# Performance work log

Hardware: AMD Instinct MI355X
Metric: run time of the kernel (lower is better)

## Reference

```python
import jax, jax.numpy as jnp
import numpy as np

B, S, D, DFF = 4, 2048, 1024, 4096


def setup_inputs() -> dict:
    key = jax.random.key(0)
    ks = jax.random.split(key, 7)
    scale = 1.0 / np.sqrt(D)
    return {
        "x": jax.random.normal(ks[0], (B, S, D), dtype=jnp.float32),
        "wq": jax.random.normal(ks[1], (D, D), dtype=jnp.float32) * scale,
        "wk": jax.random.normal(ks[2], (D, D), dtype=jnp.float32) * scale,
        "wv": jax.random.normal(ks[3], (D, D), dtype=jnp.float32) * scale,
        "wo": jax.random.normal(ks[4], (D, D), dtype=jnp.float32) * scale,
        "w1": jax.random.normal(ks[5], (D, DFF), dtype=jnp.float32) * scale,
        "w2": jax.random.normal(ks[6], (DFF, D), dtype=jnp.float32) * (1.0 / np.sqrt(DFF)),
    }


def reference(x, wq, wk, wv, wo, w1, w2):
    # Single-head attention, NO 1/sqrt(d) scaling (faithful to source).
    q = x @ wq  # [B,S,D]
    k = x @ wk
    v = x @ wv
    scores = jnp.einsum("bsd,btd->bst", q, k)  # [B,S,S]
    weights = jax.nn.softmax(scores, axis=-1)
    attn = jnp.einsum("bst,btd->bsd", weights, v)
    proj = attn @ wo
    hidden = jax.nn.relu(proj @ w1)  # [B,S,DFF]
    out = hidden @ w2
    return out + x
```

## Files before the change

kernel.cpp:

```cpp
#include <hip/hip_runtime.h>
#include <hip/hip_bf16.h>
#include <hip/hip_fp16.h>


typedef _Float16 f16;
typedef __attribute__((ext_vector_type(8))) _Float16 f16x8;
typedef __attribute__((ext_vector_type(4))) _Float16 f16x4;
typedef __attribute__((ext_vector_type(4))) float f32x4;

#define BM 128
#define BN 128
#define BK 64

__device__ inline void gload16(const void* g, void* l) {
    __builtin_amdgcn_global_load_lds(
        (const __attribute__((address_space(1))) void*)g,
        (__attribute__((address_space(3))) void*)l, 16, 0, 0);
}

template<int EPI>
__global__ __launch_bounds__(256, 2)
void gemm_f16(const f16* __restrict__ A, const f16* __restrict__ Bt,
              const float* __restrict__ Res, void* __restrict__ Cv,
              int K, int lda, int ldb, int ldc,
              long long sA, long long sB, long long sC)
{
    __shared__ char smem[32 * 1024];
    f16* Ash = (f16*)smem;
    f16* Bsh = (f16*)(smem + 16384);
    float* xbuf = (float*)smem;

    const int t = threadIdx.x;
    const int z = blockIdx.z;
    A  += (size_t)z * sA;
    Bt += (size_t)z * sB;

    const int bm0 = blockIdx.x * BM;
    const int bn0 = blockIdx.y * BN;

    const int lane = t & 63;
    const int wid  = t >> 6;
    const int quad = lane >> 4;
    const int m16  = lane & 15;
    const int ks   = wid & 1;
    const int wn64 = (wid >> 1) * 64;

    const int r0 = t >> 3;
    const int kc = ((t & 7) ^ (r0 & 7)) * 8;
    const char* gA[4]; const char* gB[4];
    #pragma unroll
    for (int i = 0; i < 4; ++i) {
        gA[i] = (const char*)(A  + (size_t)(bm0 + i * 32 + r0) * lda + kc);
        gB[i] = (const char*)(Bt + (size_t)(bn0 + i * 32 + r0) * ldb + kc);
    }
    char* lA = (char*)Ash + (wid << 10);
    char* lB = (char*)Bsh + (wid << 10);

    f32x4 acc[8][4] = {};

    const int nk = K / BK;
    #define ISSUE(kt) do { const int ko = (kt) * 128;   \
        gload16(gA[0] + ko, lA);                        \
        gload16(gA[1] + ko, lA + 4096);                 \
        gload16(gA[2] + ko, lA + 8192);                 \
        gload16(gA[3] + ko, lA + 12288);                \
        gload16(gB[0] + ko, lB);                        \
        gload16(gB[1] + ko, lB + 4096);                 \
        gload16(gB[2] + ko, lB + 8192);                 \
        gload16(gB[3] + ko, lB + 12288); } while (0)

    const int swz = m16 & 7;
    const int ha  = ((ks * 4 + quad) ^ swz) * 8;

    ISSUE(0);
    for (int kt = 0; kt < nk; ++kt) {
        __syncthreads();
        f16x8 af[8], bf[4];
        #pragma unroll
        for (int i = 0; i < 8; ++i)
            af[i] = *(const f16x8*)&Ash[(i * 16 + m16) * BK + ha];
        #pragma unroll
        for (int j = 0; j < 4; ++j)
            bf[j] = *(const f16x8*)&Bsh[(wn64 + j * 16 + m16) * BK + ha];
        __syncthreads();
        if (kt + 1 < nk) ISSUE(kt + 1);
        #pragma unroll
        for (int i = 0; i < 8; ++i)
            #pragma unroll
            for (int j = 0; j < 4; ++j)
                acc[i][j] = __builtin_amdgcn_mfma_f32_16x16x32_f16(
                                af[i], bf[j], acc[i][j], 0, 0, 0);
    }
    #undef ISSUE

    float* xb = xbuf + (wid >> 1) * 4096;
    #define XIDX(row, col) ((row) * 64 + ((col) ^ (((row) & 4) << 2)))
    if (ks == 1) {
        #pragma unroll
        for (int i = 0; i < 4; ++i)
            #pragma unroll
            for (int j = 0; j < 4; ++j)
                #pragma unroll
                for (int ri = 0; ri < 4; ++ri)
                    xb[XIDX(i * 16 + quad * 4 + ri, j * 16 + m16)] = acc[i][j][ri];
    }
    __syncthreads();
    if (ks == 0) {
        #pragma unroll
        for (int i = 0; i < 4; ++i)
            #pragma unroll
            for (int j = 0; j < 4; ++j)
                #pragma unroll
                for (int ri = 0; ri < 4; ++ri)
                    acc[i][j][ri] += xb[XIDX(i * 16 + quad * 4 + ri, j * 16 + m16)];
    }
    __syncthreads();
    if (ks == 0) {
        #pragma unroll
        for (int i = 0; i < 4; ++i)
            #pragma unroll
            for (int j = 0; j < 4; ++j)
                #pragma unroll
                for (int ri = 0; ri < 4; ++ri)
                    xb[XIDX(i * 16 + quad * 4 + ri, j * 16 + m16)] = acc[i + 4][j][ri];
    }
    __syncthreads();
    if (ks == 1) {
        #pragma unroll
        for (int i = 0; i < 4; ++i)
            #pragma unroll
            for (int j = 0; j < 4; ++j)
                #pragma unroll
                for (int ri = 0; ri < 4; ++ri)
                    acc[i + 4][j][ri] += xb[XIDX(i * 16 + quad * 4 + ri, j * 16 + m16)];
    }
    #undef XIDX

    #define STORE_TILE(IB, RB)                                                  \
        do {                                                                    \
            if (EPI <= 1) {                                                     \
                f16* C = (f16*)Cv + (size_t)z * sC;                             \
                _Pragma("unroll")                                               \
                for (int i = 0; i < 4; ++i)                                     \
                    _Pragma("unroll")                                           \
                    for (int ri = 0; ri < 4; ++ri) {                            \
                        const size_t row = (size_t)(bm0 + (RB) + i * 16 + quad * 4 + ri); \
                        f16* cp = C + row * ldc + (bn0 + wn64 + m16);           \
                        _Pragma("unroll")                                       \
                        for (int j = 0; j < 4; ++j) {                           \
                            float v = acc[(IB) + i][j][ri];                     \
                            if (EPI == 1) v = fmaxf(v, 0.0f);                   \
                            cp[j * 16] = (f16)v;                                \
                        }                                                       \
                    }                                                           \
            } else {                                                            \
                float* C = (float*)Cv + (size_t)z * sC;                         \
                _Pragma("unroll")                                               \
                for (int i = 0; i < 4; ++i)                                     \
                    _Pragma("unroll")                                           \
                    for (int ri = 0; ri < 4; ++ri) {                            \
                        const size_t row = (size_t)(bm0 + (RB) + i * 16 + quad * 4 + ri); \
                        float* cp = C + row * ldc + (bn0 + wn64 + m16);         \
                        const float* rp = (EPI == 3)                            \
                            ? Res + row * ldc + (bn0 + wn64 + m16) : nullptr;   \
                        _Pragma("unroll")                                       \
                        for (int j = 0; j < 4; ++j) {                           \
                            float v = acc[(IB) + i][j][ri];                     \
                            if (EPI == 3) v += rp[j * 16];                      \
                            cp[j * 16] = v;                                     \
                        }                                                       \
                    }                                                           \
            }                                                                   \
        } while (0)

    if (ks == 0) STORE_TILE(0, 0);
    else         STORE_TILE(4, 64);
    #undef STORE_TILE
}

__global__ __launch_bounds__(256)
void transpose_cast4(const float* __restrict__ s0, const float* __restrict__ s1,
                     const float* __restrict__ s2, const float* __restrict__ s3,
                     f16* __restrict__ d0, f16* __restrict__ d1,
                     f16* __restrict__ d2, f16* __restrict__ d3)
{
    const int R = 1024, C = 1024;
    const int z = blockIdx.z;
    const float* in = (z == 0) ? s0 : (z == 1) ? s1 : (z == 2) ? s2 : s3;
    f16* out = (z == 0) ? d0 : (z == 1) ? d1 : (z == 2) ? d2 : d3;
    __shared__ float tile[64][65];
    const int c0 = blockIdx.x * 64, r0 = blockIdx.y * 64;
    const int tc = threadIdx.x & 63, tr = threadIdx.x >> 6;
    #pragma unroll
    for (int i = 0; i < 16; ++i)
        tile[tr + i * 4][tc] = in[(size_t)(r0 + tr + i * 4) * C + c0 + tc];
    __syncthreads();
    #pragma unroll
    for (int i = 0; i < 16; ++i)
        out[(size_t)(c0 + tr + i * 4) * R + r0 + tc] = (f16)tile[tc][tr + i * 4];
}

__global__ __launch_bounds__(256)
void transpose_cast(const float* __restrict__ in, f16* __restrict__ out,
                    int R, int C)
{
    __shared__ float tile[64][65];
    const int c0 = blockIdx.x * 64, r0 = blockIdx.y * 64;
    const int tc = threadIdx.x & 63, tr = threadIdx.x >> 6;
    #pragma unroll
    for (int i = 0; i < 16; ++i)
        tile[tr + i * 4][tc] = in[(size_t)(r0 + tr + i * 4) * C + c0 + tc];
    __syncthreads();
    #pragma unroll
    for (int i = 0; i < 16; ++i)
        out[(size_t)(c0 + tr + i * 4) * R + r0 + tc] = (f16)tile[tc][tr + i * 4];
}

__global__ __launch_bounds__(256)
void cast_f16(const float* __restrict__ in, f16* __restrict__ out)
{
    const size_t i = ((size_t)blockIdx.x * 256 + threadIdx.x) * 4;
    float4 v = *(const float4*)(in + i);
    f16x4 o; o.x = (f16)v.x; o.y = (f16)v.y; o.z = (f16)v.z; o.w = (f16)v.w;
    *(f16x4*)(out + i) = o;
}

__global__ __launch_bounds__(256)
void softmax_f16(const float* __restrict__ S, f16* __restrict__ P)
{
    __shared__ float red[256];
    const float* p = S + (size_t)blockIdx.x * 2048;
    f16* q = P + (size_t)blockIdx.x * 2048;
    const int t = threadIdx.x;

    float4 u0 = *(const float4*)(p + t * 4);
    float4 u1 = *(const float4*)(p + 1024 + t * 4);

    float m = fmaxf(fmaxf(fmaxf(u0.x, u0.y), fmaxf(u0.z, u0.w)),
                    fmaxf(fmaxf(u1.x, u1.y), fmaxf(u1.z, u1.w)));
    red[t] = m;
    __syncthreads();
    #pragma unroll
    for (int s = 128; s > 0; s >>= 1) {
        if (t < s) red[t] = fmaxf(red[t], red[t + s]);
        __syncthreads();
    }
    const float rowmax = red[0];
    __syncthreads();

    u0.x = __expf(u0.x - rowmax); u0.y = __expf(u0.y - rowmax);
    u0.z = __expf(u0.z - rowmax); u0.w = __expf(u0.w - rowmax);
    u1.x = __expf(u1.x - rowmax); u1.y = __expf(u1.y - rowmax);
    u1.z = __expf(u1.z - rowmax); u1.w = __expf(u1.w - rowmax);

    red[t] = (u0.x + u0.y + u0.z + u0.w) + (u1.x + u1.y + u1.z + u1.w);
    __syncthreads();
    #pragma unroll
    for (int s = 128; s > 0; s >>= 1) {
        if (t < s) red[t] += red[t + s];
        __syncthreads();
    }
    const float inv = 1.0f / red[0];

    f16x4 o0, o1;
    o0.x = (f16)(u0.x * inv); o0.y = (f16)(u0.y * inv);
    o0.z = (f16)(u0.z * inv); o0.w = (f16)(u0.w * inv);
    o1.x = (f16)(u1.x * inv); o1.y = (f16)(u1.y * inv);
    o1.z = (f16)(u1.z * inv); o1.w = (f16)(u1.w * inv);
    *(f16x4*)(q + t * 4)        = o0;
    *(f16x4*)(q + 1024 + t * 4) = o1;
}

extern "C" void kernel_launch(void* const* d_in, const int* in_sizes, int n_in,
                              void* d_out, int out_size, void* d_ws, size_t ws_size,
                              hipStream_t stream)
{
    const float* x  = (const float*)d_in[0];
    const float* wq = (const float*)d_in[1];
    const float* wk = (const float*)d_in[2];
    const float* wv = (const float*)d_in[3];
    const float* wo = (const float*)d_in[4];
    const float* w1 = (const float*)d_in[5];
    const float* w2 = (const float*)d_in[6];
    float* out = (float*)d_out;

    const int S = 2048, D = 1024, DFF = 4096, Bb = 4;
    const int NTOK = Bb * S;

    f16* W    = (f16*)d_ws;
    f16* xh   = W;
    f16* wqkT = xh   + (size_t)NTOK * D;
    f16* wvT  = wqkT + (size_t)2 * D * D;
    f16* woT  = wvT  + (size_t)D * D;
    f16* w1T  = woT  + (size_t)D * D;
    f16* w2T  = w1T  + (size_t)D * DFF;
    f16* qk   = w2T  + (size_t)DFF * D;
    f16* vT   = qk   + (size_t)NTOK * 2 * D;
    float* sb = (float*)(vT + (size_t)D * NTOK);
    f16* ph   = qk;
    f16* at   = xh;
    f16* pj   = vT;
    f16* hd   = (f16*)sb;

    dim3 blk(256);

    cast_f16<<<dim3(NTOK * D / 1024), blk, 0, stream>>>(x, xh);
    transpose_cast4<<<dim3(D / 64, D / 64, 4), blk, 0, stream>>>(
        wq, wk, wv, wo, wqkT, wqkT + (size_t)D * D, wvT, woT);
    transpose_cast<<<dim3(DFF / 64, D / 64), blk, 0, stream>>>(w1, w1T, D, DFF);
    transpose_cast<<<dim3(D / 64, DFF / 64), blk, 0, stream>>>(w2, w2T, DFF, D);

    gemm_f16<0><<<dim3(NTOK / BM, 2 * D / BN, 1), blk, 0, stream>>>(
        xh, wqkT, nullptr, qk, D, D, D, 2 * D, 0, 0, 0);
    gemm_f16<0><<<dim3(D / BM, NTOK / BN, 1), blk, 0, stream>>>(
        wvT, xh, nullptr, vT, D, D, D, NTOK, 0, 0, 0);

    gemm_f16<2><<<dim3(S / BM, S / BN, Bb), blk, 0, stream>>>(
        qk, qk + D, nullptr, sb, D, 2 * D, 2 * D, S,
        (long long)S * 2 * D, (long long)S * 2 * D, (long long)S * S);

    softmax_f16<<<dim3(NTOK), blk, 0, stream>>>(sb, ph);

    gemm_f16<0><<<dim3(S / BM, D / BN, Bb), blk, 0, stream>>>(
        ph, vT, nullptr, at, S, S, NTOK, D,
        (long long)S * S, (long long)S, (long long)S * D);

    gemm_f16<0><<<dim3(NTOK / BM, D / BN, 1), blk, 0, stream>>>(
        at, woT, nullptr, pj, D, D, D, D, 0, 0, 0);

    gemm_f16<1><<<dim3(NTOK / BM, DFF / BN, 1), blk, 0, stream>>>(
        pj, w1T, nullptr, hd, D, D, D, DFF, 0, 0, 0);

    gemm_f16<3><<<dim3(NTOK / BM, D / BN, 1), blk, 0, stream>>>(
        hd, w2T, x, out, DFF, DFF, DFF, D, 0, 0, 0);
}
```

Measured before the change: 445.9 us.

## Add 256x256-tile GEMM kernel for QK projection, scores, and FFN up-projection

Adds a gemm_big kernel that computes a 256x256 output tile per block, with each of the four waves holding a 128x128 accumulator of 8x8 MFMA fragments. It is used for the QK projection, the attention-score GEMM and the W1 GEMM. The larger tile raises arithmetic intensity and reuse of LDS data per global load, cutting memory traffic. In exchange the kernel uses very high register pressure (256 accumulator floats per thread), runs at one block per CU, loads into a single buffer with two barriers per k-step, and launches fewer blocks, so the GPU may be under-filled.

New measurement: 450.9 us. Within noise of the previous version (+1.1%).

```diff
diff --git a/kernel.cpp b/kernel.cpp
--- a/kernel.cpp
+++ b/kernel.cpp
@@ -16,6 +16,108 @@
     __builtin_amdgcn_global_load_lds(
         (const __attribute__((address_space(1))) void*)g,
         (__attribute__((address_space(3))) void*)l, 16, 0, 0);
+}
+
+template<int EPI>
+__global__ __launch_bounds__(256, 1)
+void gemm_big(const f16* __restrict__ A, const f16* __restrict__ Bt,
+              void* __restrict__ Cv,
+              int K, int lda, int ldb, int ldc,
+              long long sA, long long sB, long long sC)
+{
+    __shared__ f16 Ash[256 * BK];
+    __shared__ f16 Bsh[256 * BK];
+
+    const int t = threadIdx.x;
+    const int z = blockIdx.z;
+    A  += (size_t)z * sA;
+    Bt += (size_t)z * sB;
+
+    const int bm0 = blockIdx.x * 256;
+    const int bn0 = blockIdx.y * 256;
+
+    const int lane = t & 63;
+    const int wid  = t >> 6;
+    const int quad = lane >> 4;
+    const int m16  = lane & 15;
+    const int wm   = (wid & 1) * 128;
+    const int wnn  = (wid >> 1) * 128;
+
+    const int r0 = t >> 3;
+    const int kc = ((t & 7) ^ (r0 & 7)) * 8;
+    const char* gA0 = (const char*)(A  + (size_t)(bm0 + r0) * lda + kc);
+    const char* gB0 = (const char*)(Bt + (size_t)(bn0 + r0) * ldb + kc);
+    const long long aStep = 64LL * lda;
+    const long long bStep = 64LL * ldb;
+    char* lA = (char*)Ash + (wid << 10);
+    char* lB = (char*)Bsh + (wid << 10);
+
+    f32x4 acc[8][8] = {};
+
+    const int nk = K / BK;
+    #define ISSUE(kt) do { const long long ko = (long long)(kt) * 128;  \
+        _Pragma("unroll")                                               \
+        for (int ii = 0; ii < 8; ++ii) {                                \
+            gload16(gA0 + ii * aStep + ko, lA + ii * 4096);             \
+            gload16(gB0 + ii * bStep + ko, lB + ii * 4096);             \
+        } } while (0)
+
+    const int swz = m16 & 7;
+
+    ISSUE(0);
+    for (int kt = 0; kt < nk; ++kt) {
+        __syncthreads();
+        f16x8 af[2][8], bf[2][8];
+        #pragma unroll
+        for (int s = 0; s < 2; ++s) {
+            const int ha = (((s << 2) | quad) ^ swz) * 8;
+            #pragma unroll
+            for (int i = 0; i < 8; ++i) {
+                af[s][i] = *(const f16x8*)&Ash[(wm + i * 16 + m16) * BK + ha];
+                bf[s][i] = *(const f16x8*)&Bsh[(wnn + i * 16 + m16) * BK + ha];
+            }
+        }
+        __syncthreads();
+        if (kt + 1 < nk) ISSUE(kt + 1);
+        #pragma unroll
+        for (int s = 0; s < 2; ++s)
+            #pragma unroll
+            for (int i = 0; i < 8; ++i)
+                #pragma unroll
+                for (int j = 0; j < 8; ++j)
+                    acc[i][j] = __builtin_amdgcn_mfma_f32_16x16x32_f16(
+                                    af[s][i], bf[s][j], acc[i][j], 0, 0, 0);
+    }
+    #undef ISSUE
+
+    if (EPI <= 1) {
+        f16* C = (f16*)Cv + (size_t)z * sC;
+        #pragma unroll
+        for (int i = 0; i < 8; ++i)
+            #pragma unroll
+            for (int ri = 0; ri < 4; ++ri) {
+                const size_t row = (size_t)(bm0 + wm + i * 16 + quad * 4 + ri);
+                f16* cp = C + row * ldc + (bn0 + wnn + m16);
+                #pragma unroll
+                for (int j = 0; j < 8; ++j) {
+                    float v = acc[i][j][ri];
+                    if (EPI == 1) v = fmaxf(v, 0.0f);
+                    cp[j * 16] = (f16)v;
+                }
+            }
+    } else {
+        float* C = (float*)Cv + (size_t)z * sC;
+        #pragma unroll
+        for (int i = 0; i < 8; ++i)
+            #pragma unroll
+            for (int ri = 0; ri < 4; ++ri) {
+                const size_t row = (size_t)(bm0 + wm + i * 16 + quad * 4 + ri);
+                float* cp = C + row * ldc + (bn0 + wnn + m16);
+                #pragma unroll
+                for (int j = 0; j < 8; ++j)
+                    cp[j * 16] = acc[i][j][ri];
+            }
+    }
 }
 
 template<int EPI>
@@ -310,13 +412,13 @@
     transpose_cast<<<dim3(DFF / 64, D / 64), blk, 0, stream>>>(w1, w1T, D, DFF);
     transpose_cast<<<dim3(D / 64, DFF / 64), blk, 0, stream>>>(w2, w2T, DFF, D);
 
-    gemm_f16<0><<<dim3(NTOK / BM, 2 * D / BN, 1), blk, 0, stream>>>(
-        xh, wqkT, nullptr, qk, D, D, D, 2 * D, 0, 0, 0);
+    gemm_big<0><<<dim3(NTOK / 256, 2 * D / 256, 1), blk, 0, stream>>>(
+        xh, wqkT, qk, D, D, D, 2 * D, 0, 0, 0);
     gemm_f16<0><<<dim3(D / BM, NTOK / BN, 1), blk, 0, stream>>>(
         wvT, xh, nullptr, vT, D, D, D, NTOK, 0, 0, 0);
 
-    gemm_f16<2><<<dim3(S / BM, S / BN, Bb), blk, 0, stream>>>(
-        qk, qk + D, nullptr, sb, D, 2 * D, 2 * D, S,
+    gemm_big<2><<<dim3(S / 256, S / 256, Bb), blk, 0, stream>>>(
+        qk, qk + D, sb, D, 2 * D, 2 * D, S,
         (long long)S * 2 * D, (long long)S * 2 * D, (long long)S * S);
 
     softmax_f16<<<dim3(NTOK), blk, 0, stream>>>(sb, ph);
@@ -328,8 +430,8 @@
     gemm_f16<0><<<dim3(NTOK / BM, D / BN, 1), blk, 0, stream>>>(
         at, woT, nullptr, pj, D, D, D, D, 0, 0, 0);
 
-    gemm_f16<1><<<dim3(NTOK / BM, DFF / BN, 1), blk, 0, stream>>>(
-        pj, w1T, nullptr, hd, D, D, D, DFF, 0, 0, 0);
+    gemm_big<1><<<dim3(NTOK / 256, DFF / 256, 1), blk, 0, stream>>>(
+        pj, w1T, hd, D, D, D, DFF, 0, 0, 0);
 
     gemm_f16<3><<<dim3(NTOK / BM, D / BN, 1), blk, 0, stream>>>(
         hd, w2T, x, out, DFF, DFF, DFF, D, 0, 0, 0);
```
